# Optimization experiments

Hardware: AMD Instinct MI355X
Metric: run time of the kernel (lower is better)

## Reference

```python
import jax, jax.numpy as jnp
import numpy as np

# NTU-25 joint groupings (0-indexed)
BODY_GROUP = [np.array([5,6,7,8,22,23])-1, np.array([9,10,11,12,24,25])-1,
              np.array([13,14,15,16])-1, np.array([17,18,19,20])-1,
              np.array([1,2,3,4,21])-1]
PART_GROUP = [np.array([1,2,21])-1, np.array([3,4])-1, np.array([5,6,7])-1,
              np.array([8,22,23])-1, np.array([9,10,11])-1, np.array([12,24,25])-1,
              np.array([13,14])-1, np.array([15,16])-1, np.array([17,18])-1,
              np.array([19,20])-1]

def _corr_joints(parts):
    num_joints = max(max(p) for p in parts) + 1
    res = []
    for i in range(num_joints):
        for j, p in enumerate(parts):
            if i in p:
                res.append(j)
                break
    return np.asarray(res, dtype=np.int32)

JOINTS_PART = _corr_joints(PART_GROUP)  # [25] -> part id in [0,10)
JOINTS_BODY = _corr_joints(BODY_GROUP)  # [25] -> body id in [0,5)

N, C, T, V, S = 64, 96, 128, 25, 3

def setup_inputs() -> dict:
    key = jax.random.key(0)
    ks = jax.random.split(key, 10)
    x = jax.random.normal(ks[0], (N, C, T, V), jnp.float32)
    p_att = jax.random.normal(ks[1], (N, S, 10, 10), jnp.float32)
    b_att = jax.random.normal(ks[2], (N, S, 5, 5), jnp.float32)
    w_in = jax.random.normal(ks[3], (3 * C, C), jnp.float32) * (1.0 / np.sqrt(C))
    b_in = jax.random.normal(ks[4], (3 * C,), jnp.float32) * 0.01
    w_ff = jax.random.normal(ks[5], (C, C), jnp.float32) * (1.0 / np.sqrt(C))
    b_ff = jax.random.normal(ks[6], (C,), jnp.float32) * 0.01
    bn_gamma = jnp.ones((C,), jnp.float32)
    bn_beta = jnp.zeros((C,), jnp.float32)
    bn_mean = jnp.zeros((C,), jnp.float32)
    bn_var = jnp.ones((C,), jnp.float32)
    return {"x": x, "p_att": p_att, "b_att": b_att, "w_in": w_in, "b_in": b_in,
            "w_ff": w_ff, "b_ff": b_ff, "bn_gamma": bn_gamma, "bn_beta": bn_beta,
            "bn_mean": bn_mean, "bn_var": bn_var}

def reference(x, p_att, b_att, w_in, b_in, w_ff, b_ff, bn_gamma, bn_beta, bn_mean, bn_var):
    n, c, t, v = x.shape
    s = S
    mid = c // s
    jp = jnp.asarray(JOINTS_PART)
    jb = jnp.asarray(JOINTS_BODY)
    # 1x1 conv -> QKV: [N, 3C, T, V] viewed as [N, 3, S, mid, T, V]
    qkv = jnp.einsum('nctv,oc->notv', x, w_in) + b_in[None, :, None, None]
    qkv = qkv.reshape(n, 3, s, mid, t, v)
    q, k, val = qkv[:, 0], qkv[:, 1], qkv[:, 2]
    att = jnp.tanh(jnp.einsum('nsctu,nsctv->nsuv', q, k) / (mid * t))
    # structured gather of part/body biases to joint-level [N,S,V,V]
    pp = p_att[:, :, jp[:, None], jp[None, :]]
    bb = b_att[:, :, jb[:, None], jb[None, :]]
    att = att + pp + bb
    y = jnp.einsum('nsuv,nsctv->nsctu', att, val).reshape(n, c, t, v)
    # ff_nets: 1x1 conv + BatchNorm (eval mode, running stats)
    y = jnp.einsum('nctv,oc->notv', y, w_ff) + b_ff[None, :, None, None]
    inv = bn_gamma / jnp.sqrt(bn_var + 1e-5)
    y = (y - bn_mean[None, :, None, None]) * inv[None, :, None, None] + bn_beta[None, :, None, None]
    return jax.nn.leaky_relu(x + y, 0.1)
```

## Files before the change

kernel.cpp:

```cpp
#include <hip/hip_runtime.h>
#include <cmath>

#define NN 64
#define CC 96
#define TT 128
#define VV 25
#define SS 3
#define TB 4
#define NTB (TT/TB)
#define ROWS (TB*VV)
#define XTP 104
#define XTROWS 112
#define QKP 200
#define QKROWS 112
#define VALP 40
#define YLP 104

typedef __attribute__((ext_vector_type(8))) __bf16 bf16x8;
typedef __attribute__((ext_vector_type(4))) float f32x4;

#define MFMA16(a,b,c) __builtin_amdgcn_mfma_f32_16x16x32_bf16((a),(b),(c),0,0,0)

__constant__ int JP[25] = {0,0,1,1,2,2,2,3,4,4,4,5,6,6,7,7,8,8,9,9,0,3,3,5,5};
__constant__ int JB[25] = {4,4,4,4,0,0,0,0,1,1,1,1,2,2,2,2,3,3,3,3,4,0,0,1,1};

__device__ inline unsigned short f2b(float f) {
  unsigned int u = __float_as_uint(f);
  u += 0x7fffu + ((u >> 16) & 1u);
  return (unsigned short)(u >> 16);
}
__device__ inline float b2f(unsigned short h) {
  return __uint_as_float(((unsigned int)h) << 16);
}
__device__ inline bf16x8 ldbf8(const unsigned short* p) {
  union { uint4 u; bf16x8 b; } z;
  z.u = *(const uint4*)p;
  return z.b;
}
__device__ inline f32x4 fz() {
  f32x4 z; z[0] = 0.f; z[1] = 0.f; z[2] = 0.f; z[3] = 0.f; return z;
}

__global__ __launch_bounds__(256) void k0(
    const float* __restrict__ w_in, const float* __restrict__ w_ff,
    const float* __restrict__ b_ff, const float* __restrict__ gam,
    const float* __restrict__ bet, const float* __restrict__ mea,
    const float* __restrict__ var,
    unsigned short* __restrict__ wbin, unsigned short* __restrict__ wbff,
    float* __restrict__ scsh)
{
  int i = blockIdx.x * 256 + threadIdx.x;
  if (i < 288 * 96) wbin[i] = f2b(w_in[i]);
  if (i < 96 * 96)  wbff[i] = f2b(w_ff[i]);
  if (i < 96) {
    float sc = gam[i] * rsqrtf(var[i] + 1e-5f);
    scsh[i]      = sc;
    scsh[96 + i] = (b_ff[i] - mea[i]) * sc + bet[i];
  }
}

__global__ __launch_bounds__(256, 2) void k1(
    const float* __restrict__ x, const unsigned short* __restrict__ wbin,
    const float* __restrict__ b_in, float* __restrict__ partG)
{
  __shared__ unsigned short xT[XTROWS * XTP];
  __shared__ unsigned short qk[QKROWS * QKP];

  const int tid  = threadIdx.x;
  const int wid  = tid >> 6, lane = tid & 63;
  const int lrow = lane & 15;
  const int lk8  = (lane >> 4) << 3;
  const int ldr4 = (lane >> 4) << 2;
  const int tb = blockIdx.x & (NTB - 1);
  const int n  = blockIdx.x >> 5;
  const int t0 = tb * TB;

  const float* xb = x + (size_t)n * CC * TT * VV + (size_t)t0 * VV;
  for (int e = tid; e < CC * (ROWS / 4); e += 256) {
    int i4 = e % (ROWS / 4), c = e / (ROWS / 4);
    float4 xv = *(const float4*)&xb[(size_t)c * TT * VV + i4 * 4];
    int i0 = i4 * 4;
    xT[(i0    ) * XTP + c] = f2b(xv.x);
    xT[(i0 + 1) * XTP + c] = f2b(xv.y);
    xT[(i0 + 2) * XTP + c] = f2b(xv.z);
    xT[(i0 + 3) * XTP + c] = f2b(xv.w);
  }
  __syncthreads();

  f32x4 acc[3][7];
  #pragma unroll
  for (int i = 0; i < 3; ++i)
    #pragma unroll
    for (int nf = 0; nf < 7; ++nf) acc[i][nf] = fz();

  #pragma unroll
  for (int ks = 0; ks < 3; ++ks) {
    bf16x8 a[3];
    #pragma unroll
    for (int i = 0; i < 3; ++i)
      a[i] = ldbf8(&wbin[((wid * 3 + i) * 16 + lrow) * 96 + ks * 32 + lk8]);
    #pragma unroll
    for (int nf = 0; nf < 7; ++nf) {
      bf16x8 b = ldbf8(&xT[(nf * 16 + lrow) * XTP + ks * 32 + lk8]);
      #pragma unroll
      for (int i = 0; i < 3; ++i)
        acc[i][nf] = MFMA16(a[i], b, acc[i][nf]);
    }
  }
  #pragma unroll
  for (int i = 0; i < 3; ++i) {
    int ob = (wid * 3 + i) * 16 + ldr4;
    float4 bb = *(const float4*)&b_in[ob];
    #pragma unroll
    for (int nf = 0; nf < 7; ++nf) {
      int col = nf * 16 + lrow;
      ushort4 h;
      h.x = f2b(acc[i][nf][0] + bb.x);
      h.y = f2b(acc[i][nf][1] + bb.y);
      h.z = f2b(acc[i][nf][2] + bb.z);
      h.w = f2b(acc[i][nf][3] + bb.w);
      *(ushort4*)&qk[col * QKP + ob] = h;
    }
  }
  __syncthreads();

  if (wid < 3) {
    const int s = wid;
    f32x4 g[2][2];
    g[0][0] = fz(); g[0][1] = fz(); g[1][0] = fz(); g[1][1] = fz();
    #pragma unroll
    for (int dt = 0; dt < TB; ++dt) {
      int r0 = dt * VV;
      bf16x8 a0 = ldbf8(&qk[(r0 + lrow) * QKP + s * 32 + lk8]);
      bf16x8 a1 = ldbf8(&qk[(r0 + 16 + lrow) * QKP + s * 32 + lk8]);
      bf16x8 b0 = ldbf8(&qk[(r0 + lrow) * QKP + 96 + s * 32 + lk8]);
      bf16x8 b1 = ldbf8(&qk[(r0 + 16 + lrow) * QKP + 96 + s * 32 + lk8]);
      g[0][0] = MFMA16(a0, b0, g[0][0]);
      g[0][1] = MFMA16(a0, b1, g[0][1]);
      g[1][0] = MFMA16(a1, b0, g[1][0]);
      g[1][1] = MFMA16(a1, b1, g[1][1]);
    }
    float* pg = partG + ((size_t)(n * SS + s) * NTB + tb) * (VV * VV);
    #pragma unroll
    for (int mi = 0; mi < 2; ++mi)
      #pragma unroll
      for (int ni = 0; ni < 2; ++ni)
        #pragma unroll
        for (int r = 0; r < 4; ++r) {
          int u = mi * 16 + ldr4 + r, v = ni * 16 + lrow;
          if (u < VV && v < VV) pg[u * VV + v] = g[mi][ni][r];
        }
  }
}

__global__ __launch_bounds__(256) void k2(
    const float* __restrict__ partG, const float* __restrict__ p_att,
    const float* __restrict__ b_att, unsigned short* __restrict__ att)
{
  const int ns = blockIdx.x;
  for (int e = threadIdx.x; e < 1024; e += 256) {
    int u = e >> 5, v = e & 31;
    float a = 0.f;
    if (u < VV && v < VV) {
      float g = 0.f;
      const float* pg = partG + (size_t)ns * NTB * (VV * VV) + u * VV + v;
      for (int tb = 0; tb < NTB; ++tb) g += pg[tb * VV * VV];
      a = tanhf(g * (1.0f / 4096.0f))
        + p_att[(size_t)ns * 100 + JP[u] * 10 + JP[v]]
        + b_att[(size_t)ns * 25  + JB[u] * 5  + JB[v]];
    }
    att[(size_t)ns * 1024 + e] = f2b(a);
  }
}

__global__ __launch_bounds__(256, 4) void k3(
    const float* __restrict__ x, const unsigned short* __restrict__ wbin,
    const unsigned short* __restrict__ wbff,
    const float* __restrict__ b_in, const float* __restrict__ scsh,
    const unsigned short* __restrict__ att, float* __restrict__ out)
{
  __shared__ unsigned short xT[XTROWS * XTP];
  __shared__ unsigned short val[384 * VALP];

  const int tid  = threadIdx.x;
  const int wid  = tid >> 6, lane = tid & 63;
  const int lrow = lane & 15;
  const int lk8  = (lane >> 4) << 3;
  const int ldr4 = (lane >> 4) << 2;
  const int tb = blockIdx.x & (NTB - 1);
  const int n  = blockIdx.x >> 5;
  const int t0 = tb * TB;

  const float* xb = x + (size_t)n * CC * TT * VV + (size_t)t0 * VV;
  for (int e = tid; e < CC * (ROWS / 4); e += 256) {
    int i4 = e % (ROWS / 4), c = e / (ROWS / 4);
    float4 xv = *(const float4*)&xb[(size_t)c * TT * VV + i4 * 4];
    int i0 = i4 * 4;
    xT[(i0    ) * XTP + c] = f2b(xv.x);
    xT[(i0 + 1) * XTP + c] = f2b(xv.y);
    xT[(i0 + 2) * XTP + c] = f2b(xv.z);
    xT[(i0 + 3) * XTP + c] = f2b(xv.w);
  }
  {
    uint4 z; z.x = 0u; z.y = 0u; z.z = 0u; z.w = 0u;
    for (int e = tid; e < 384; e += 256)
      *(uint4*)&val[e * VALP + 24] = z;
  }
  __syncthreads();

  for (int nf = wid * 2; nf < 7 && nf < wid * 2 + 2; ++nf) {
    f32x4 acc[6];
    #pragma unroll
    for (int mf = 0; mf < 6; ++mf) acc[mf] = fz();
    #pragma unroll
    for (int ks = 0; ks < 3; ++ks) {
      bf16x8 b = ldbf8(&xT[(nf * 16 + lrow) * XTP + ks * 32 + lk8]);
      #pragma unroll
      for (int mf = 0; mf < 6; ++mf) {
        bf16x8 a = ldbf8(&wbin[(192 + mf * 16 + lrow) * 96 + ks * 32 + lk8]);
        acc[mf] = MFMA16(a, b, acc[mf]);
      }
    }
    int col = nf * 16 + lrow;
    if (col < ROWS) {
      int dt = col / VV, v = col - dt * VV;
      #pragma unroll
      for (int mf = 0; mf < 6; ++mf) {
        float4 bb = *(const float4*)&b_in[192 + mf * 16 + ldr4];
        const float* bp = (const float*)&bb;
        #pragma unroll
        for (int r = 0; r < 4; ++r) {
          int c = mf * 16 + ldr4 + r;
          val[(dt * 96 + c) * VALP + v] = f2b(acc[mf][r] + bp[r]);
        }
      }
    }
  }
  __syncthreads();

  const unsigned short* attn = att + (size_t)(n * SS) * 1024;
  f32x4 y[3][2][2];
  #pragma unroll
  for (int s = 0; s < 3; ++s)
    #pragma unroll
    for (int mi = 0; mi < 2; ++mi)
      #pragma unroll
      for (int ci = 0; ci < 2; ++ci) y[s][mi][ci] = fz();

  #pragma unroll
  for (int s = 0; s < 3; ++s) {
    bf16x8 b[2];
    #pragma unroll
    for (int ci = 0; ci < 2; ++ci) {
      int col = (wid * 2 + ci) * 16 + lrow;
      int dt = col >> 5, cm = col & 31;
      b[ci] = ldbf8(&val[(dt * 96 + s * 32 + cm) * VALP + lk8]);
    }
    #pragma unroll
    for (int mi = 0; mi < 2; ++mi) {
      bf16x8 a = ldbf8(&attn[(size_t)s * 1024 + (mi * 16 + lrow) * 32 + lk8]);
      #pragma unroll
      for (int ci = 0; ci < 2; ++ci)
        y[s][mi][ci] = MFMA16(a, b[ci], y[s][mi][ci]);
    }
  }
  __syncthreads();

  unsigned short* yL = val;
  #pragma unroll
  for (int s = 0; s < 3; ++s)
    #pragma unroll
    for (int mi = 0; mi < 2; ++mi)
      #pragma unroll
      for (int ci = 0; ci < 2; ++ci) {
        int col = (wid * 2 + ci) * 16 + lrow;
        int dt = col >> 5, cm = col & 31;
        int c = s * 32 + cm;
        #pragma unroll
        for (int r = 0; r < 4; ++r) {
          int u = mi * 16 + ldr4 + r;
          if (u < VV) yL[(dt * VV + u) * YLP + c] = f2b(y[s][mi][ci][r]);
        }
      }
  __syncthreads();

  for (int nf = wid * 2; nf < 7 && nf < wid * 2 + 2; ++nf) {
    f32x4 acc[6];
    #pragma unroll
    for (int mf = 0; mf < 6; ++mf) acc[mf] = fz();
    #pragma unroll
    for (int ks = 0; ks < 3; ++ks) {
      bf16x8 b = ldbf8(&yL[(nf * 16 + lrow) * YLP + ks * 32 + lk8]);
      #pragma unroll
      for (int mf = 0; mf < 6; ++mf) {
        bf16x8 a = ldbf8(&wbff[(mf * 16 + lrow) * 96 + ks * 32 + lk8]);
        acc[mf] = MFMA16(a, b, acc[mf]);
      }
    }
    int i = nf * 16 + lrow;
    if (i < ROWS) {
      int dt = i / VV, u = i - dt * VV;
      int t = t0 + dt;
      #pragma unroll
      for (int mf = 0; mf < 6; ++mf) {
        int o0 = mf * 16 + ldr4;
        ushort4 xr = *(const ushort4*)&xT[i * XTP + o0];
        float4 sc = *(const float4*)&scsh[o0];
        float4 sh = *(const float4*)&scsh[96 + o0];
        float zr[4];
        zr[0] = acc[mf][0] * sc.x + sh.x + b2f(xr.x);
        zr[1] = acc[mf][1] * sc.y + sh.y + b2f(xr.y);
        zr[2] = acc[mf][2] * sc.z + sh.z + b2f(xr.z);
        zr[3] = acc[mf][3] * sc.w + sh.w + b2f(xr.w);
        #pragma unroll
        for (int r = 0; r < 4; ++r) {
          float z = zr[r];
          z = (z >= 0.f) ? z : 0.1f * z;
          out[((size_t)(n * CC + o0 + r) * TT + t) * VV + u] = z;
        }
      }
    }
  }
}

extern "C" void kernel_launch(void* const* d_in, const int* in_sizes, int n_in,
                              void* d_out, int out_size, void* d_ws, size_t ws_size,
                              hipStream_t stream)
{
  const float* x     = (const float*)d_in[0];
  const float* p_att = (const float*)d_in[1];
  const float* b_att = (const float*)d_in[2];
  const float* w_in  = (const float*)d_in[3];
  const float* b_in  = (const float*)d_in[4];
  const float* w_ff  = (const float*)d_in[5];
  const float* b_ff  = (const float*)d_in[6];
  const float* gam   = (const float*)d_in[7];
  const float* bet   = (const float*)d_in[8];
  const float* mea   = (const float*)d_in[9];
  const float* var   = (const float*)d_in[10];
  float* out = (float*)d_out;

  char* ws = (char*)d_ws;
  unsigned short* wbin = (unsigned short*)ws;
  unsigned short* wbff = wbin + 288 * 96;
  unsigned short* attw = wbff + 96 * 96;
  float* scsh  = (float*)(ws + 466944);
  float* partG = (float*)(ws + 467712);

  k0<<<108, 256, 0, stream>>>(w_in, w_ff, b_ff, gam, bet, mea, var,
                              wbin, wbff, scsh);
  k1<<<NN * NTB, 256, 0, stream>>>(x, wbin, b_in, partG);
  k2<<<NN * SS, 256, 0, stream>>>(partG, p_att, b_att, attw);
  k3<<<NN * NTB, 256, 0, stream>>>(x, wbin, wbff, b_in, scsh, attw, out);
}
```

Before: 143.8 us.

## Halve k3 time tile to two frames and switch x staging to scalar loads

```diff
diff --git a/kernel.cpp b/kernel.cpp
--- a/kernel.cpp
+++ b/kernel.cpp
@@ -6,13 +6,19 @@
 #define TT 128
 #define VV 25
 #define SS 3
+
 #define TB 4
 #define NTB (TT/TB)
 #define ROWS (TB*VV)
+#define XTROWS 112
+
+#define TB3 2
+#define NTB3 (TT/TB3)
+#define ROWS3 (TB3*VV)
+#define XTROWS3 64
+
 #define XTP 104
-#define XTROWS 112
 #define QKP 200
-#define QKROWS 112
 #define VALP 40
 #define YLP 104
 
@@ -64,7 +70,8 @@
     const float* __restrict__ b_in, float* __restrict__ partG)
 {
   __shared__ unsigned short xT[XTROWS * XTP];
-  __shared__ unsigned short qk[QKROWS * QKP];
+  __shared__ unsigned short qk[XTROWS * QKP];
+  __shared__ float bL[192];
 
   const int tid  = threadIdx.x;
   const int wid  = tid >> 6, lane = tid & 63;
@@ -76,15 +83,11 @@
   const int t0 = tb * TB;
 
   const float* xb = x + (size_t)n * CC * TT * VV + (size_t)t0 * VV;
-  for (int e = tid; e < CC * (ROWS / 4); e += 256) {
-    int i4 = e % (ROWS / 4), c = e / (ROWS / 4);
-    float4 xv = *(const float4*)&xb[(size_t)c * TT * VV + i4 * 4];
-    int i0 = i4 * 4;
-    xT[(i0    ) * XTP + c] = f2b(xv.x);
-    xT[(i0 + 1) * XTP + c] = f2b(xv.y);
-    xT[(i0 + 2) * XTP + c] = f2b(xv.z);
-    xT[(i0 + 3) * XTP + c] = f2b(xv.w);
-  }
+  for (int e = tid; e < CC * ROWS; e += 256) {
+    int i = e / CC, c = e - i * CC;
+    xT[i * XTP + c] = f2b(xb[(size_t)c * TT * VV + i]);
+  }
+  if (tid < 192) bL[tid] = b_in[tid];
   __syncthreads();
 
   f32x4 acc[3][7];
@@ -110,7 +113,7 @@
   #pragma unroll
   for (int i = 0; i < 3; ++i) {
     int ob = (wid * 3 + i) * 16 + ldr4;
-    float4 bb = *(const float4*)&b_in[ob];
+    float4 bb = *(const float4*)&bL[ob];
     #pragma unroll
     for (int nf = 0; nf < 7; ++nf) {
       int col = nf * 16 + lrow;
@@ -173,56 +176,51 @@
   }
 }
 
-__global__ __launch_bounds__(256, 4) void k3(
+__global__ __launch_bounds__(256, 2) void k3(
     const float* __restrict__ x, const unsigned short* __restrict__ wbin,
     const unsigned short* __restrict__ wbff,
     const float* __restrict__ b_in, const float* __restrict__ scsh,
     const unsigned short* __restrict__ att, float* __restrict__ out)
 {
-  __shared__ unsigned short xT[XTROWS * XTP];
-  __shared__ unsigned short val[384 * VALP];
+  __shared__ unsigned short xT[XTROWS3 * XTP];
+  __shared__ unsigned short val[192 * VALP];
 
   const int tid  = threadIdx.x;
   const int wid  = tid >> 6, lane = tid & 63;
   const int lrow = lane & 15;
   const int lk8  = (lane >> 4) << 3;
   const int ldr4 = (lane >> 4) << 2;
-  const int tb = blockIdx.x & (NTB - 1);
-  const int n  = blockIdx.x >> 5;
-  const int t0 = tb * TB;
+  const int tb = blockIdx.x & (NTB3 - 1);
+  const int n  = blockIdx.x >> 6;
+  const int t0 = tb * TB3;
 
   const float* xb = x + (size_t)n * CC * TT * VV + (size_t)t0 * VV;
-  for (int e = tid; e < CC * (ROWS / 4); e += 256) {
-    int i4 = e % (ROWS / 4), c = e / (ROWS / 4);
-    float4 xv = *(const float4*)&xb[(size_t)c * TT * VV + i4 * 4];
-    int i0 = i4 * 4;
-    xT[(i0    ) * XTP + c] = f2b(xv.x);
-    xT[(i0 + 1) * XTP + c] = f2b(xv.y);
-    xT[(i0 + 2) * XTP + c] = f2b(xv.z);
-    xT[(i0 + 3) * XTP + c] = f2b(xv.w);
+  for (int e = tid; e < CC * ROWS3; e += 256) {
+    int i = e / CC, c = e - i * CC;
+    xT[i * XTP + c] = f2b(xb[(size_t)c * TT * VV + i]);
   }
   {
     uint4 z; z.x = 0u; z.y = 0u; z.z = 0u; z.w = 0u;
-    for (int e = tid; e < 384; e += 256)
+    for (int e = tid; e < 192; e += 256)
       *(uint4*)&val[e * VALP + 24] = z;
   }
   __syncthreads();
 
-  for (int nf = wid * 2; nf < 7 && nf < wid * 2 + 2; ++nf) {
+  {
     f32x4 acc[6];
     #pragma unroll
     for (int mf = 0; mf < 6; ++mf) acc[mf] = fz();
     #pragma unroll
     for (int ks = 0; ks < 3; ++ks) {
-      bf16x8 b = ldbf8(&xT[(nf * 16 + lrow) * XTP + ks * 32 + lk8]);
+      bf16x8 b = ldbf8(&xT[(wid * 16 + lrow) * XTP + ks * 32 + lk8]);
       #pragma unroll
       for (int mf = 0; mf < 6; ++mf) {
         bf16x8 a = ldbf8(&wbin[(192 + mf * 16 + lrow) * 96 + ks * 32 + lk8]);
         acc[mf] = MFMA16(a, b, acc[mf]);
       }
     }
-    int col = nf * 16 + lrow;
-    if (col < ROWS) {
+    int col = wid * 16 + lrow;
+    if (col < ROWS3) {
       int dt = col / VV, v = col - dt * VV;
       #pragma unroll
       for (int mf = 0; mf < 6; ++mf) {
@@ -239,66 +237,58 @@
   __syncthreads();
 
   const unsigned short* attn = att + (size_t)(n * SS) * 1024;
-  f32x4 y[3][2][2];
+  f32x4 y[3][2];
   #pragma unroll
-  for (int s = 0; s < 3; ++s)
-    #pragma unroll
-    for (int mi = 0; mi < 2; ++mi)
-      #pragma unroll
-      for (int ci = 0; ci < 2; ++ci) y[s][mi][ci] = fz();
-
-  #pragma unroll
-  for (int s = 0; s < 3; ++s) {
-    bf16x8 b[2];
-    #pragma unroll
-    for (int ci = 0; ci < 2; ++ci) {
-      int col = (wid * 2 + ci) * 16 + lrow;
-      int dt = col >> 5, cm = col & 31;
-      b[ci] = ldbf8(&val[(dt * 96 + s * 32 + cm) * VALP + lk8]);
-    }
-    #pragma unroll
-    for (int mi = 0; mi < 2; ++mi) {
-      bf16x8 a = ldbf8(&attn[(size_t)s * 1024 + (mi * 16 + lrow) * 32 + lk8]);
-      #pragma unroll
-      for (int ci = 0; ci < 2; ++ci)
-        y[s][mi][ci] = MFMA16(a, b[ci], y[s][mi][ci]);
+  for (int s = 0; s < 3; ++s) { y[s][0] = fz(); y[s][1] = fz(); }
+
+  {
+    const int col = wid * 16 + lrow;
+    const int dt = col >> 5, cm = col & 31;
+    #pragma unroll
+    for (int s = 0; s < 3; ++s) {
+      bf16x8 b = ldbf8(&val[(dt * 96 + s * 32 + cm) * VALP + lk8]);
+      #pragma unroll
+      for (int mi = 0; mi < 2; ++mi) {
+        bf16x8 a = ldbf8(&attn[(size_t)s * 1024 + (mi * 16 + lrow) * 32 + lk8]);
+        y[s][mi] = MFMA16(a, b, y[s][mi]);
+      }
     }
   }
   __syncthreads();
 
   unsigned short* yL = val;
-  #pragma unroll
-  for (int s = 0; s < 3; ++s)
-    #pragma unroll
-    for (int mi = 0; mi < 2; ++mi)
-      #pragma unroll
-      for (int ci = 0; ci < 2; ++ci) {
-        int col = (wid * 2 + ci) * 16 + lrow;
-        int dt = col >> 5, cm = col & 31;
-        int c = s * 32 + cm;
+  {
+    const int col = wid * 16 + lrow;
+    const int dt = col >> 5, cm = col & 31;
+    #pragma unroll
+    for (int s = 0; s < 3; ++s) {
+      const int c = s * 32 + cm;
+      #pragma unroll
+      for (int mi = 0; mi < 2; ++mi)
         #pragma unroll
         for (int r = 0; r < 4; ++r) {
           int u = mi * 16 + ldr4 + r;
-          if (u < VV) yL[(dt * VV + u) * YLP + c] = f2b(y[s][mi][ci][r]);
+          if (u < VV) yL[(dt * VV + u) * YLP + c] = f2b(y[s][mi][r]);
         }
-      }
-  __syncthreads();
-
-  for (int nf = wid * 2; nf < 7 && nf < wid * 2 + 2; ++nf) {
+    }
+  }
+  __syncthreads();
+
+  {
     f32x4 acc[6];
     #pragma unroll
     for (int mf = 0; mf < 6; ++mf) acc[mf] = fz();
     #pragma unroll
     for (int ks = 0; ks < 3; ++ks) {
-      bf16x8 b = ldbf8(&yL[(nf * 16 + lrow) * YLP + ks * 32 + lk8]);
+      bf16x8 b = ldbf8(&yL[(wid * 16 + lrow) * YLP + ks * 32 + lk8]);
       #pragma unroll
       for (int mf = 0; mf < 6; ++mf) {
         bf16x8 a = ldbf8(&wbff[(mf * 16 + lrow) * 96 + ks * 32 + lk8]);
         acc[mf] = MFMA16(a, b, acc[mf]);
       }
     }
-    int i = nf * 16 + lrow;
-    if (i < ROWS) {
+    int i = wid * 16 + lrow;
+    if (i < ROWS3) {
       int dt = i / VV, u = i - dt * VV;
       int t = t0 + dt;
       #pragma unroll
@@ -351,5 +341,5 @@
                               wbin, wbff, scsh);
   k1<<<NN * NTB, 256, 0, stream>>>(x, wbin, b_in, partG);
   k2<<<NN * SS, 256, 0, stream>>>(partG, p_att, b_att, attw);
-  k3<<<NN * NTB, 256, 0, stream>>>(x, wbin, wbff, b_in, scsh, attw, out);
-}
+  k3<<<NN * NTB3, 256, 0, stream>>>(x, wbin, wbff, b_in, scsh, attw, out);
+}
```

New measurement: 168.9 us. 1.17x slower.

## Stage x transpose through shared scratch and reorder partial Gram layout

Applied to the files above, without the earlier changes.

```diff
diff --git a/kernel.cpp b/kernel.cpp
--- a/kernel.cpp
+++ b/kernel.cpp
@@ -9,10 +9,11 @@
 #define TB 4
 #define NTB (TT/TB)
 #define ROWS (TB*VV)
+#define XTROWS 112
+
 #define XTP 104
-#define XTROWS 112
+#define XFP 104
 #define QKP 200
-#define QKROWS 112
 #define VALP 40
 #define YLP 104
 
@@ -59,12 +60,39 @@
   }
 }
 
+__device__ inline void stageA(const float* __restrict__ xb,
+                              unsigned short* __restrict__ xf, int tid)
+{
+  for (int e = tid; e < CC * (ROWS / 4); e += 256) {
+    int i4 = e % (ROWS / 4), c = e / (ROWS / 4);
+    float4 v = *(const float4*)&xb[(size_t)c * (TT * VV) + i4 * 4];
+    ushort4 h;
+    h.x = f2b(v.x); h.y = f2b(v.y); h.z = f2b(v.z); h.w = f2b(v.w);
+    *(ushort4*)&xf[c * XFP + i4 * 4] = h;
+  }
+}
+__device__ inline void stageB(const unsigned short* __restrict__ xf,
+                              unsigned short* __restrict__ xT, int tid)
+{
+  for (int e = tid; e < ROWS * (CC / 4); e += 256) {
+    int i = e % ROWS, c4 = e / ROWS;
+    ushort4 h;
+    h.x = xf[(c4 * 4 + 0) * XFP + i];
+    h.y = xf[(c4 * 4 + 1) * XFP + i];
+    h.z = xf[(c4 * 4 + 2) * XFP + i];
+    h.w = xf[(c4 * 4 + 3) * XFP + i];
+    *(ushort4*)&xT[i * XTP + c4 * 4] = h;
+  }
+}
+
 __global__ __launch_bounds__(256, 2) void k1(
     const float* __restrict__ x, const unsigned short* __restrict__ wbin,
     const float* __restrict__ b_in, float* __restrict__ partG)
 {
-  __shared__ unsigned short xT[XTROWS * XTP];
-  __shared__ unsigned short qk[QKROWS * QKP];
+  __shared__ __align__(16) unsigned short xT[XTROWS * XTP];
+  __shared__ __align__(16) unsigned short qk[XTROWS * QKP];
+  __shared__ float bL[192];
+  unsigned short* xf = qk;
 
   const int tid  = threadIdx.x;
   const int wid  = tid >> 6, lane = tid & 63;
@@ -76,15 +104,10 @@
   const int t0 = tb * TB;
 
   const float* xb = x + (size_t)n * CC * TT * VV + (size_t)t0 * VV;
-  for (int e = tid; e < CC * (ROWS / 4); e += 256) {
-    int i4 = e % (ROWS / 4), c = e / (ROWS / 4);
-    float4 xv = *(const float4*)&xb[(size_t)c * TT * VV + i4 * 4];
-    int i0 = i4 * 4;
-    xT[(i0    ) * XTP + c] = f2b(xv.x);
-    xT[(i0 + 1) * XTP + c] = f2b(xv.y);
-    xT[(i0 + 2) * XTP + c] = f2b(xv.z);
-    xT[(i0 + 3) * XTP + c] = f2b(xv.w);
-  }
+  stageA(xb, xf, tid);
+  if (tid < 192) bL[tid] = b_in[tid];
+  __syncthreads();
+  stageB(xf, xT, tid);
   __syncthreads();
 
   f32x4 acc[3][7];
@@ -110,7 +133,7 @@
   #pragma unroll
   for (int i = 0; i < 3; ++i) {
     int ob = (wid * 3 + i) * 16 + ldr4;
-    float4 bb = *(const float4*)&b_in[ob];
+    float4 bb = *(const float4*)&bL[ob];
     #pragma unroll
     for (int nf = 0; nf < 7; ++nf) {
       int col = nf * 16 + lrow;
@@ -140,7 +163,7 @@
       g[1][0] = MFMA16(a1, b0, g[1][0]);
       g[1][1] = MFMA16(a1, b1, g[1][1]);
     }
-    float* pg = partG + ((size_t)(n * SS + s) * NTB + tb) * (VV * VV);
+    float* pg = partG + ((size_t)tb * (NN * SS) + (n * SS + s)) * (VV * VV);
     #pragma unroll
     for (int mi = 0; mi < 2; ++mi)
       #pragma unroll
@@ -163,8 +186,9 @@
     float a = 0.f;
     if (u < VV && v < VV) {
       float g = 0.f;
-      const float* pg = partG + (size_t)ns * NTB * (VV * VV) + u * VV + v;
-      for (int tb = 0; tb < NTB; ++tb) g += pg[tb * VV * VV];
+      #pragma unroll 4
+      for (int tb = 0; tb < NTB; ++tb)
+        g += partG[((size_t)tb * (NN * SS) + ns) * (VV * VV) + u * VV + v];
       a = tanhf(g * (1.0f / 4096.0f))
         + p_att[(size_t)ns * 100 + JP[u] * 10 + JP[v]]
         + b_att[(size_t)ns * 25  + JB[u] * 5  + JB[v]];
@@ -173,14 +197,15 @@
   }
 }
 
-__global__ __launch_bounds__(256, 4) void k3(
+__global__ __launch_bounds__(256, 2) void k3(
     const float* __restrict__ x, const unsigned short* __restrict__ wbin,
     const unsigned short* __restrict__ wbff,
     const float* __restrict__ b_in, const float* __restrict__ scsh,
     const unsigned short* __restrict__ att, float* __restrict__ out)
 {
-  __shared__ unsigned short xT[XTROWS * XTP];
-  __shared__ unsigned short val[384 * VALP];
+  __shared__ __align__(16) unsigned short xT[XTROWS * XTP];
+  __shared__ __align__(16) unsigned short val[384 * VALP];
+  unsigned short* xf = val;
 
   const int tid  = threadIdx.x;
   const int wid  = tid >> 6, lane = tid & 63;
@@ -192,15 +217,10 @@
   const int t0 = tb * TB;
 
   const float* xb = x + (size_t)n * CC * TT * VV + (size_t)t0 * VV;
-  for (int e = tid; e < CC * (ROWS / 4); e += 256) {
-    int i4 = e % (ROWS / 4), c = e / (ROWS / 4);
-    float4 xv = *(const float4*)&xb[(size_t)c * TT * VV + i4 * 4];
-    int i0 = i4 * 4;
-    xT[(i0    ) * XTP + c] = f2b(xv.x);
-    xT[(i0 + 1) * XTP + c] = f2b(xv.y);
-    xT[(i0 + 2) * XTP + c] = f2b(xv.z);
-    xT[(i0 + 3) * XTP + c] = f2b(xv.w);
-  }
+  stageA(xb, xf, tid);
+  __syncthreads();
+  stageB(xf, xT, tid);
+  __syncthreads();
   {
     uint4 z; z.x = 0u; z.y = 0u; z.z = 0u; z.w = 0u;
     for (int e = tid; e < 384; e += 256)
```

Result: faster. 127.8 us (-11.2%).
